# Performance work log

Measured on AMD Instinct MI355X. Metric: run time of the kernel, lower is better.

The kernel has to match this reference:

```python
import jax, jax.numpy as jnp
import numpy as np

B, S1, S2, H, OPC = 256, 512, 64, 768, 64
NEG = -1e12


def setup_inputs() -> dict:
    key = jax.random.key(0)
    ks = jax.random.split(key, 20)
    sc = 0.02
    d = {
        "current_emb": jax.random.normal(ks[0], (B, H), jnp.float32),
        "left_emb": jax.random.normal(ks[1], (B, H), jnp.float32),
        "encoder_outputs": jax.random.normal(ks[2], (B, S1, H), jnp.float32),
        "var_pades": jax.random.normal(ks[3], (B, S2, H), jnp.float32),
        "emb_op_const": jax.random.normal(ks[4], (OPC, H), jnp.float32),
        "W_l": jax.random.normal(ks[5], (H, H), jnp.float32) * sc,
        "b_l": jnp.zeros((H,), jnp.float32),
        "W_lg": jax.random.normal(ks[6], (H, H), jnp.float32) * sc,
        "b_lg": jnp.zeros((H,), jnp.float32),
        "W_r": jax.random.normal(ks[7], (2 * H, H), jnp.float32) * sc,
        "b_r": jnp.zeros((H,), jnp.float32),
        "W_rg": jax.random.normal(ks[8], (2 * H, H), jnp.float32) * sc,
        "b_rg": jnp.zeros((H,), jnp.float32),
        "W_attn": jax.random.normal(ks[9], (2 * H, H), jnp.float32) * sc,
        "b_attn": jnp.zeros((H,), jnp.float32),
        "v_attn": jax.random.normal(ks[10], (H,), jnp.float32) * sc,
        "W_score": jax.random.normal(ks[11], (3 * H, H), jnp.float32) * sc,
        "b_score": jnp.zeros((H,), jnp.float32),
        "v_score": jax.random.normal(ks[12], (H,), jnp.float32) * sc,
        "has_left": jax.random.randint(ks[13], (B,), 0, 2, jnp.int32),
        "source_mask": jax.random.randint(ks[14], (B, S1), 0, 2, jnp.int32),
        "candi_mask": jax.random.randint(ks[15], (B, OPC + S2), 0, 2, jnp.int32),
    }
    return d


def reference(current_emb, left_emb, encoder_outputs, var_pades, emb_op_const,
              W_l, b_l, W_lg, b_lg, W_r, b_r, W_rg, b_rg,
              W_attn, b_attn, v_attn, W_score, b_score, v_score,
              has_left, source_mask, candi_mask):
    # --- gated tree combine (two branches, selected per sample by has_left) ---
    g_l = jnp.tanh(current_emb @ W_l + b_l)
    t_l = jax.nn.sigmoid(current_emb @ W_lg + b_lg)
    lc = jnp.concatenate([left_emb, current_emb], axis=1)          # [B, 2H]
    g_r = jnp.tanh(lc @ W_r + b_r)
    t_r = jax.nn.sigmoid(lc @ W_rg + b_rg)
    node = jnp.where(has_left[:, None].astype(bool), g_r * t_r, g_l * t_l)  # [B, H]

    # --- additive attention over encoder outputs ---
    Bn, S, Hn = encoder_outputs.shape
    hid = jnp.broadcast_to(node[:, None, :], (Bn, S, Hn))
    energy = jnp.tanh(jnp.concatenate([hid, encoder_outputs], -1) @ W_attn + b_attn) @ v_attn  # [B, S]
    energy = jnp.where(source_mask.astype(bool), NEG, energy)
    attn = jax.nn.softmax(energy, axis=1)
    context = jnp.einsum('bs,bsh->bh', attn, encoder_outputs)      # [B, H]

    # --- leaf score over op/const/var candidates ---
    leaf = jnp.concatenate([node, context], axis=-1)               # [B, 2H]
    emb_all = jnp.concatenate(
        [jnp.broadcast_to(emb_op_const[None], (Bn,) + emb_op_const.shape), var_pades], axis=1)  # [B, O, H]
    O = emb_all.shape[1]
    sc_in = jnp.concatenate(
        [jnp.broadcast_to(leaf[:, None, :], (Bn, O, 2 * Hn)), emb_all], axis=-1)  # [B, O, 3H]
    score = jnp.tanh(sc_in @ W_score + b_score) @ v_score          # [B, O]
    num_score = jnp.where(candi_mask.astype(bool), NEG, score)
    return num_score, node[:, None, :], context[:, None, :], emb_all
```

## Files before the change

### kernel.cpp

```cpp
#include <hip/hip_runtime.h>
#include <math.h>

constexpr int Bq  = 256;
constexpr int S1q = 512;
constexpr int S2q = 64;
constexpr int Hq  = 768;
constexpr int OPCq = 64;
constexpr int OTq  = 128;
#define NEGq (-1e12f)

typedef unsigned int   u32;
typedef unsigned short u16;


__device__ __forceinline__ float fast_tanh(float x) {
    x = fminf(fmaxf(x, -15.f), 15.f);
    float e = __expf(2.f * x);
    return (e - 1.f) / (e + 1.f);
}
__device__ __forceinline__ float fast_sigmoid(float x) {
    x = fminf(fmaxf(x, -30.f), 30.f);
    return 1.f / (1.f + __expf(-x));
}

__device__ __forceinline__ u16 bf16_rne(float x) {
    union { float f; u32 u; } c; c.f = x;
    return (u16)((c.u + 0x7fffu + ((c.u >> 16) & 1u)) >> 16);
}
__device__ __forceinline__ float bf16_f(u16 h) {
    union { u32 u; float f; } c; c.u = ((u32)h) << 16; return c.f;
}

typedef __attribute__((ext_vector_type(8))) short bf16x8_t;
typedef __attribute__((ext_vector_type(4))) float f32x4_t;
#define MFMA16 __builtin_amdgcn_mfma_f32_16x16x32_bf16

template <int BT>
__global__ __launch_bounds__(256)
void node_kernel(const float* __restrict__ cur_emb, const float* __restrict__ left_emb,
                 const float* __restrict__ W_l,  const float* __restrict__ b_l,
                 const float* __restrict__ W_lg, const float* __restrict__ b_lg,
                 const float* __restrict__ W_r,  const float* __restrict__ b_r,
                 const float* __restrict__ W_rg, const float* __restrict__ b_rg,
                 const int* __restrict__ has_left, float* __restrict__ node_out) {
    __shared__ float lcs[BT][2 * Hq];
    const int tid = threadIdx.x;
    const int h  = blockIdx.x * 256 + tid;
    const int b0 = blockIdx.y * BT;
    for (int idx = tid; idx < BT * Hq; idx += 256) {
        int j = idx / Hq, k = idx % Hq;
        lcs[j][k]      = left_emb[(b0 + j) * Hq + k];
        lcs[j][Hq + k] = cur_emb[(b0 + j) * Hq + k];
    }
    __syncthreads();
    float agl[BT], atl[BT], agr[BT], atr[BT];
#pragma unroll
    for (int j = 0; j < BT; j++) { agl[j] = b_l[h]; atl[j] = b_lg[h]; agr[j] = b_r[h]; atr[j] = b_rg[h]; }
    for (int k = 0; k < Hq; k++) {
        float wl = W_l[k * Hq + h], wlg = W_lg[k * Hq + h];
#pragma unroll
        for (int j = 0; j < BT; j++) { float x = lcs[j][Hq + k]; agl[j] += x * wl; atl[j] += x * wlg; }
    }
    for (int k = 0; k < 2 * Hq; k++) {
        float wr = W_r[k * Hq + h], wrg = W_rg[k * Hq + h];
#pragma unroll
        for (int j = 0; j < BT; j++) { float x = lcs[j][k]; agr[j] += x * wr; atr[j] += x * wrg; }
    }
#pragma unroll
    for (int j = 0; j < BT; j++) {
        int b = b0 + j;
        float n = has_left[b] ? fast_tanh(agr[j]) * fast_sigmoid(atr[j])
                              : fast_tanh(agl[j]) * fast_sigmoid(atl[j]);
        node_out[b * Hq + h] = n;
    }
}

template <int BT>
__global__ __launch_bounds__(256)
void proj_kernel(const float* __restrict__ A1, const float* __restrict__ A2,
                 int K1, int K2,
                 const float* __restrict__ W, const float* __restrict__ bias,
                 float* __restrict__ out) {
    __shared__ float As[BT][2 * Hq];
    const int tid = threadIdx.x;
    const int h  = blockIdx.x * 256 + tid;
    const int b0 = blockIdx.y * BT;
    const int K = K1 + K2;
    for (int idx = tid; idx < BT * K1; idx += 256) {
        int j = idx / K1, k = idx % K1;
        As[j][k] = A1[(b0 + j) * K1 + k];
    }
    if (A2) {
        for (int idx = tid; idx < BT * K2; idx += 256) {
            int j = idx / K2, k = idx % K2;
            As[j][K1 + k] = A2[(b0 + j) * K2 + k];
        }
    }
    __syncthreads();
    float acc[BT];
#pragma unroll
    for (int j = 0; j < BT; j++) acc[j] = bias ? bias[h] : 0.f;
    for (int k = 0; k < K; k++) {
        float w = W[k * Hq + h];
#pragma unroll
        for (int j = 0; j < BT; j++) acc[j] += As[j][k] * w;
    }
#pragma unroll
    for (int j = 0; j < BT; j++) out[(b0 + j) * Hq + h] = acc[j];
}

__global__ __launch_bounds__(256)
void w_prep_kernel(const float* __restrict__ W,
                   uint4* __restrict__ Wf_hi, uint4* __restrict__ Wf_lo) {
    __shared__ float tile[64][65];
    const int tid = threadIdx.x;
    const int k0 = blockIdx.x * 64, n0 = blockIdx.y * 64;
    const int tx = tid & 63, tyy = tid >> 6;
    for (int u = tyy; u < 64; u += 4)
        tile[u][tx] = W[(size_t)(k0 + u) * Hq + n0 + tx];
    __syncthreads();
    const int l15 = tid & 15, lg = (tid >> 4) & 3, ktl = (tid >> 6) & 1;
    for (int c16 = tid >> 7; c16 < 4; c16 += 2) {
        const int kl = ktl * 32 + lg * 8;
        const int nl = c16 * 16 + l15;
        u32 h[4], l[4];
#pragma unroll
        for (int p = 0; p < 4; p++) {
            float a = tile[kl + 2 * p][nl], b = tile[kl + 2 * p + 1][nl];
            u16 ha = bf16_rne(a), hb = bf16_rne(b);
            u16 la = bf16_rne(a - bf16_f(ha)), lb = bf16_rne(b - bf16_f(hb));
            h[p] = (u32)ha | ((u32)hb << 16);
            l[p] = (u32)la | ((u32)lb << 16);
        }
        size_t idx = ((size_t)((n0 >> 4) + c16) * 24 + (k0 >> 5) + ktl) * 64 + lg * 16 + l15;
        Wf_hi[idx] = make_uint4(h[0], h[1], h[2], h[3]);
        Wf_lo[idx] = make_uint4(l[0], l[1], l[2], l[3]);
    }
}

__global__ __launch_bounds__(512)
void fused_tanh_dot_mfma(const float* __restrict__ A,
                         const uint4* __restrict__ Wf_hi,
                         const uint4* __restrict__ Wf_lo,
                         const float* __restrict__ addv,
                         const float* __restrict__ vvec,
                         float* __restrict__ out,
                         const int* __restrict__ maskp,
                         int shift, int ostride, int ooff) {
    __shared__ __align__(16) u16 Ah[128 * 32];
    __shared__ __align__(16) u16 Al[128 * 32];
    __shared__ float part[4][128];
    const int tid  = threadIdx.x;
    const int lane = tid & 63;
    const int wid  = tid >> 6, wr = wid >> 2, wc = wid & 3;
    const int l15  = lane & 15, lg = lane >> 4;
    const int rowbase = blockIdx.x * 128;

    part[tid >> 7][tid & 127] = 0.f;

    const int srow = tid >> 2, sk = (tid & 3) * 8;
    const float* Arow = A + (size_t)(rowbase + srow) * Hq + sk;

    const int bw = (rowbase + wr * 64) >> shift;
    const float* ad = addv + (size_t)bw * Hq;
    const int arow0 = wr * 64 + l15;

    for (int ct = 0; ct < 3; ct++) {
        f32x4_t acc[4][4];
#pragma unroll
        for (int i = 0; i < 4; i++)
#pragma unroll
            for (int j = 0; j < 4; j++) acc[i][j] = (f32x4_t){0.f, 0.f, 0.f, 0.f};

        const int c0 = ct * 16 + wc * 4;
        float4 f0 = *(const float4*)(Arow);
        float4 f1 = *(const float4*)(Arow + 4);
        for (int kt = 0; kt < 24; kt++) {
            float4 n0 = f0, n1 = f1;
            if (kt < 23) {
                n0 = *(const float4*)(Arow + (kt + 1) * 32);
                n1 = *(const float4*)(Arow + (kt + 1) * 32 + 4);
            }
            __syncthreads();
            {
                float xs[8] = {f0.x, f0.y, f0.z, f0.w, f1.x, f1.y, f1.z, f1.w};
                u32 h[4], l[4];
#pragma unroll
                for (int p = 0; p < 4; p++) {
                    u16 ha = bf16_rne(xs[2 * p]), hb = bf16_rne(xs[2 * p + 1]);
                    u16 la = bf16_rne(xs[2 * p] - bf16_f(ha));
                    u16 lb = bf16_rne(xs[2 * p + 1] - bf16_f(hb));
                    h[p] = (u32)ha | ((u32)hb << 16);
                    l[p] = (u32)la | ((u32)lb << 16);
                }
                *(uint4*)&Ah[srow * 32 + sk] = make_uint4(h[0], h[1], h[2], h[3]);
                *(uint4*)&Al[srow * 32 + sk] = make_uint4(l[0], l[1], l[2], l[3]);
            }
            __syncthreads();

            bf16x8_t ahf[4], alf[4];
#pragma unroll
            for (int i = 0; i < 4; i++) {
                ahf[i] = *(const bf16x8_t*)&Ah[(arow0 + i * 16) * 32 + lg * 8];
                alf[i] = *(const bf16x8_t*)&Al[(arow0 + i * 16) * 32 + lg * 8];
            }
#pragma unroll
            for (int j = 0; j < 4; j++) {
                uint4 wh4 = Wf_hi[((size_t)(c0 + j) * 24 + kt) * 64 + lane];
                uint4 wl4 = Wf_lo[((size_t)(c0 + j) * 24 + kt) * 64 + lane];
                bf16x8_t wh = *(bf16x8_t*)&wh4;
                bf16x8_t wl = *(bf16x8_t*)&wl4;
#pragma unroll
                for (int i = 0; i < 4; i++) {
                    acc[i][j] = MFMA16(ahf[i], wh, acc[i][j], 0, 0, 0);
                    acc[i][j] = MFMA16(alf[i], wh, acc[i][j], 0, 0, 0);
                    acc[i][j] = MFMA16(ahf[i], wl, acc[i][j], 0, 0, 0);
                }
            }
            f0 = n0; f1 = n1;
        }

        float sacc[4][4];
#pragma unroll
        for (int i = 0; i < 4; i++)
#pragma unroll
            for (int r = 0; r < 4; r++) sacc[i][r] = 0.f;
#pragma unroll
        for (int j = 0; j < 4; j++) {
            const int col = ct * 256 + wc * 64 + j * 16 + l15;
            const float vv = vvec[col];
            const float av = ad[col];
#pragma unroll
            for (int i = 0; i < 4; i++)
#pragma unroll
                for (int r = 0; r < 4; r++)
                    sacc[i][r] += vv * fast_tanh(acc[i][j][r] + av);
        }
#pragma unroll
        for (int i = 0; i < 4; i++)
#pragma unroll
            for (int r = 0; r < 4; r++) {
                float s = sacc[i][r];
                s += __shfl_xor(s, 1);
                s += __shfl_xor(s, 2);
                s += __shfl_xor(s, 4);
                s += __shfl_xor(s, 8);
                if (l15 == 0) {
                    part[wc][wr * 64 + i * 16 + lg * 4 + r] += s;
                }
            }
    }
    __syncthreads();
    if (tid < 128) {
        int grow = rowbase + tid;
        int b = grow >> shift;
        int j = grow - (b << shift);
        int oidx = b * ostride + ooff + j;
        float val = part[0][tid] + part[1][tid] + part[2][tid] + part[3][tid];
        if (maskp && maskp[oidx]) val = NEGq;
        out[oidx] = val;
    }
}

__global__ __launch_bounds__(256)
void softmax_kernel(float* __restrict__ e, const int* __restrict__ smask) {
    __shared__ float red[256];
    const int b = blockIdx.x, tid = threadIdx.x;
    float e0 = e[b * S1q + tid], e1 = e[b * S1q + 256 + tid];
    if (smask[b * S1q + tid]) e0 = NEGq;
    if (smask[b * S1q + 256 + tid]) e1 = NEGq;
    red[tid] = fmaxf(e0, e1);
    __syncthreads();
    for (int off = 128; off > 0; off >>= 1) {
        if (tid < off) red[tid] = fmaxf(red[tid], red[tid + off]);
        __syncthreads();
    }
    float mx = red[0];
    __syncthreads();
    float p0 = __expf(e0 - mx), p1 = __expf(e1 - mx);
    red[tid] = p0 + p1;
    __syncthreads();
    for (int off = 128; off > 0; off >>= 1) {
        if (tid < off) red[tid] += red[tid + off];
        __syncthreads();
    }
    float inv = 1.f / red[0];
    e[b * S1q + tid] = p0 * inv;
    e[b * S1q + 256 + tid] = p1 * inv;
}

__global__ __launch_bounds__(256)
void context_kernel(const float* __restrict__ attn, const float* __restrict__ enc,
                    float* __restrict__ ctx_out) {
    __shared__ float attn_s[S1q];
    const int tid = threadIdx.x;
    const int b = blockIdx.y;
    const int h = blockIdx.x * 256 + tid;
    attn_s[tid]       = attn[b * S1q + tid];
    attn_s[256 + tid] = attn[b * S1q + 256 + tid];
    __syncthreads();
    float c = 0.f;
    const float* ep = enc + (size_t)b * S1q * Hq + h;
    for (int s = 0; s < S1q; s++) c += attn_s[s] * ep[(size_t)s * Hq];
    ctx_out[b * Hq + h] = c;
}

__global__ __launch_bounds__(256)
void opscore_kernel(const float* __restrict__ scorebase, const float* __restrict__ opproj,
                    const float* __restrict__ vsc, const int* __restrict__ cmask,
                    float* __restrict__ num_score) {
    __shared__ float sb[Hq];
    __shared__ float red[256];
    const int b = blockIdx.x, tid = threadIdx.x;
    for (int i = tid; i < Hq; i += 256) sb[i] = scorebase[b * Hq + i];
    __syncthreads();
    const int o = tid & 63, q = tid >> 6;
    float partl = 0.f;
    for (int h = q * 192; h < (q + 1) * 192; h++)
        partl += vsc[h] * fast_tanh(sb[h] + opproj[o * Hq + h]);
    red[tid] = partl;
    __syncthreads();
    if (tid < 64) {
        float val = red[tid] + red[tid + 64] + red[tid + 128] + red[tid + 192];
        int oidx = b * OTq + tid;
        num_score[oidx] = cmask[oidx] ? NEGq : val;
    }
}

__global__ __launch_bounds__(256)
void emb_all_kernel(const float* __restrict__ opc, const float* __restrict__ var,
                    float4* __restrict__ out) {
    const long long total = (long long)Bq * OTq * (Hq / 4);
    for (long long idx = (long long)blockIdx.x * 256 + threadIdx.x; idx < total;
         idx += (long long)gridDim.x * 256) {
        long long b = idx / (OTq * (Hq / 4));
        int rem = (int)(idx - b * (OTq * (Hq / 4)));
        int o = rem / (Hq / 4), hv = rem % (Hq / 4);
        float4 val;
        if (o < OPCq) val = *(const float4*)&opc[o * Hq + hv * 4];
        else          val = *(const float4*)&var[((b * S2q) + (o - OPCq)) * (long long)Hq + hv * 4];
        out[idx] = val;
    }
}

extern "C" void kernel_launch(void* const* d_in, const int* in_sizes, int n_in,
                              void* d_out, int out_size, void* d_ws, size_t ws_size,
                              hipStream_t stream) {
    const float* cur     = (const float*)d_in[0];
    const float* left    = (const float*)d_in[1];
    const float* enc     = (const float*)d_in[2];
    const float* var     = (const float*)d_in[3];
    const float* opc     = (const float*)d_in[4];
    const float* W_l     = (const float*)d_in[5];
    const float* b_l     = (const float*)d_in[6];
    const float* W_lg    = (const float*)d_in[7];
    const float* b_lg    = (const float*)d_in[8];
    const float* W_r     = (const float*)d_in[9];
    const float* b_r     = (const float*)d_in[10];
    const float* W_rg    = (const float*)d_in[11];
    const float* b_rg    = (const float*)d_in[12];
    const float* W_attn  = (const float*)d_in[13];
    const float* b_attn  = (const float*)d_in[14];
    const float* v_attn  = (const float*)d_in[15];
    const float* W_score = (const float*)d_in[16];
    const float* b_score = (const float*)d_in[17];
    const float* v_score = (const float*)d_in[18];
    const int*   has_left= (const int*)d_in[19];
    const int*   smask   = (const int*)d_in[20];
    const int*   cmask   = (const int*)d_in[21];

    float* out       = (float*)d_out;
    float* num_score = out;
    float* node      = out + 32768;
    float* context   = out + 229376;
    float* emb_all   = out + 425984;

    float* ws        = (float*)d_ws;
    float* nodeproj  = ws;
    float* energy    = ws + 196608;
    float* scorebase = ws + 196608 + 131072;
    float* opproj    = scorebase + 196608;

    uint4* Wf_attn_hi = (uint4*)emb_all;
    uint4* Wf_attn_lo = Wf_attn_hi + 73728;
    uint4* Wf_sc_hi   = Wf_attn_lo + 73728;
    uint4* Wf_sc_lo   = Wf_sc_hi + 73728;

    w_prep_kernel<<<dim3(12, 12), 256, 0, stream>>>(W_attn + (size_t)768 * Hq,
                                                    Wf_attn_hi, Wf_attn_lo);
    w_prep_kernel<<<dim3(12, 12), 256, 0, stream>>>(W_score + (size_t)1536 * Hq,
                                                    Wf_sc_hi, Wf_sc_lo);
    node_kernel<8><<<dim3(3, 32), 256, 0, stream>>>(cur, left, W_l, b_l, W_lg, b_lg,
                                                    W_r, b_r, W_rg, b_rg, has_left, node);
    proj_kernel<8><<<dim3(3, 32), 256, 0, stream>>>(node, nullptr, 768, 0, W_attn, b_attn, nodeproj);
    proj_kernel<8><<<dim3(3, 8), 256, 0, stream>>>(opc, nullptr, 768, 0,
                                                   W_score + (size_t)1536 * Hq, nullptr, opproj);
    fused_tanh_dot_mfma<<<1024, 512, 0, stream>>>(enc, Wf_attn_hi, Wf_attn_lo, nodeproj,
                                                  v_attn, energy, nullptr, 9, S1q, 0);
    softmax_kernel<<<256, 256, 0, stream>>>(energy, smask);
    context_kernel<<<dim3(3, 256), 256, 0, stream>>>(energy, enc, context);
    proj_kernel<8><<<dim3(3, 32), 256, 0, stream>>>(node, context, 768, 768, W_score, b_score, scorebase);
    fused_tanh_dot_mfma<<<128, 512, 0, stream>>>(var, Wf_sc_hi, Wf_sc_lo, scorebase,
                                                 v_score, num_score, cmask, 6, OTq, OPCq);
    opscore_kernel<<<256, 256, 0, stream>>>(scorebase, opproj, v_score, cmask, num_score);
    emb_all_kernel<<<4096, 256, 0, stream>>>(opc, var, (float4*)emb_all);
}
```

Baseline: 2.087 ms.

## Restructure fused MFMA kernel: full-N per block, double-buffered LDS, vectorized context/opscore

The fused tanh-dot MFMA kernel now has each warp keep accumulators for all of its output columns in one pass instead of looping three column tiles. This means activation rows are loaded and split to bf16 hi/lo once rather than three times. LDS staging is double-buffered with one barrier per k-step, and a template picks the row/column warp split, so the score pass uses 64-row blocks across 256 blocks. The context kernel is rewritten to use float4 loads with a sequence split plus a shared-memory reduction, and the opscore kernel is rewritten to use per-warp shuffle reductions with coalesced opproj reads. The larger accumulator arrays (24 f32x4 per lane) increase register pressure and may limit occupancy.

```diff
diff --git a/kernel.cpp b/kernel.cpp
--- a/kernel.cpp
+++ b/kernel.cpp
@@ -34,6 +34,21 @@
 typedef __attribute__((ext_vector_type(8))) short bf16x8_t;
 typedef __attribute__((ext_vector_type(4))) float f32x4_t;
 #define MFMA16 __builtin_amdgcn_mfma_f32_16x16x32_bf16
+
+__device__ __forceinline__ void cvt_store8(float4 f0, float4 f1, u16* ph, u16* pl) {
+    float xs[8] = {f0.x, f0.y, f0.z, f0.w, f1.x, f1.y, f1.z, f1.w};
+    u32 h[4], l[4];
+#pragma unroll
+    for (int p = 0; p < 4; p++) {
+        u16 ha = bf16_rne(xs[2 * p]), hb = bf16_rne(xs[2 * p + 1]);
+        u16 la = bf16_rne(xs[2 * p] - bf16_f(ha));
+        u16 lb = bf16_rne(xs[2 * p + 1] - bf16_f(hb));
+        h[p] = (u32)ha | ((u32)hb << 16);
+        l[p] = (u32)la | ((u32)lb << 16);
+    }
+    *(uint4*)ph = make_uint4(h[0], h[1], h[2], h[3]);
+    *(uint4*)pl = make_uint4(l[0], l[1], l[2], l[3]);
+}
 
 template <int BT>
 __global__ __launch_bounds__(256)
@@ -138,7 +153,8 @@
     }
 }
 
-__global__ __launch_bounds__(512)
+template <int NWR>
+__global__ __launch_bounds__(512, 2)
 void fused_tanh_dot_mfma(const float* __restrict__ A,
                          const uint4* __restrict__ Wf_hi,
                          const uint4* __restrict__ Wf_lo,
@@ -147,116 +163,131 @@
                          float* __restrict__ out,
                          const int* __restrict__ maskp,
                          int shift, int ostride, int ooff) {
-    __shared__ __align__(16) u16 Ah[128 * 32];
-    __shared__ __align__(16) u16 Al[128 * 32];
-    __shared__ float part[4][128];
+    constexpr int NWC  = 8 / NWR;
+    constexpr int J16  = 6 * NWR;
+    constexpr int ROWS = NWR * 64;
+    __shared__ __align__(16) u16 AhL[2][ROWS * 32];
+    __shared__ __align__(16) u16 AlL[2][ROWS * 32];
+    __shared__ float part[NWC * ROWS];
+
     const int tid  = threadIdx.x;
     const int lane = tid & 63;
-    const int wid  = tid >> 6, wr = wid >> 2, wc = wid & 3;
+    const int wid  = tid >> 6;
+    const int wr   = wid / NWC, wc = wid % NWC;
     const int l15  = lane & 15, lg = lane >> 4;
-    const int rowbase = blockIdx.x * 128;
-
-    part[tid >> 7][tid & 127] = 0.f;
-
-    const int srow = tid >> 2, sk = (tid & 3) * 8;
-    const float* Arow = A + (size_t)(rowbase + srow) * Hq + sk;
+    const int rowbase = blockIdx.x * ROWS;
+
+    const bool st_act = (NWR == 2) || (tid < 256);
+    const int sg = ((tid >> 6) * 4 + (tid & 3)) * 16 + ((tid >> 2) & 15);
+    const float* Aptr = A + (size_t)(rowbase + (tid >> 2)) * Hq + (tid & 3) * 8;
 
     const int bw = (rowbase + wr * 64) >> shift;
     const float* ad = addv + (size_t)bw * Hq;
-    const int arow0 = wr * 64 + l15;
-
-    for (int ct = 0; ct < 3; ct++) {
-        f32x4_t acc[4][4];
+    const int c0 = wc * J16;
+    const uint4* whb = Wf_hi + (size_t)c0 * 24 * 64 + lane;
+    const uint4* wlb = Wf_lo + (size_t)c0 * 24 * 64 + lane;
+    const int ag = (wr * 4) * 64 + lg * 16 + l15;
+
+    f32x4_t acc[4][J16];
+#pragma unroll
+    for (int i = 0; i < 4; i++)
+#pragma unroll
+        for (int j = 0; j < J16; j++) acc[i][j] = (f32x4_t){0.f, 0.f, 0.f, 0.f};
+
+    if (st_act) {
+        float4 f0 = *(const float4*)(Aptr);
+        float4 f1 = *(const float4*)(Aptr + 4);
+        cvt_store8(f0, f1, &AhL[0][sg * 8], &AlL[0][sg * 8]);
+    }
+    __syncthreads();
+
+    for (int kt = 0; kt < 24; ++kt) {
+        const int cur = kt & 1;
+        float4 f0 = {0.f, 0.f, 0.f, 0.f}, f1 = {0.f, 0.f, 0.f, 0.f};
+        if (st_act && kt < 23) {
+            f0 = *(const float4*)(Aptr + (kt + 1) * 32);
+            f1 = *(const float4*)(Aptr + (kt + 1) * 32 + 4);
+        }
+        const u16* AhC = AhL[cur];
+        const u16* AlC = AlL[cur];
+        {
+            bf16x8_t a0h = *(const bf16x8_t*)&AhC[(ag + 0 * 64) * 8];
+            bf16x8_t a1h = *(const bf16x8_t*)&AhC[(ag + 1 * 64) * 8];
+            bf16x8_t a0l = *(const bf16x8_t*)&AlC[(ag + 0 * 64) * 8];
+            bf16x8_t a1l = *(const bf16x8_t*)&AlC[(ag + 1 * 64) * 8];
+#pragma unroll
+            for (int j = 0; j < J16; j++) {
+                uint4 h4 = whb[((size_t)j * 24 + kt) * 64];
+                uint4 l4 = wlb[((size_t)j * 24 + kt) * 64];
+                bf16x8_t wh = *(bf16x8_t*)&h4, wl = *(bf16x8_t*)&l4;
+                acc[0][j] = MFMA16(a0h, wh, acc[0][j], 0, 0, 0);
+                acc[0][j] = MFMA16(a0l, wh, acc[0][j], 0, 0, 0);
+                acc[0][j] = MFMA16(a0h, wl, acc[0][j], 0, 0, 0);
+                acc[1][j] = MFMA16(a1h, wh, acc[1][j], 0, 0, 0);
+                acc[1][j] = MFMA16(a1l, wh, acc[1][j], 0, 0, 0);
+                acc[1][j] = MFMA16(a1h, wl, acc[1][j], 0, 0, 0);
+            }
+        }
+        {
+            bf16x8_t a2h = *(const bf16x8_t*)&AhC[(ag + 2 * 64) * 8];
+            bf16x8_t a3h = *(const bf16x8_t*)&AhC[(ag + 3 * 64) * 8];
+            bf16x8_t a2l = *(const bf16x8_t*)&AlC[(ag + 2 * 64) * 8];
+            bf16x8_t a3l = *(const bf16x8_t*)&AlC[(ag + 3 * 64) * 8];
+#pragma unroll
+            for (int j = 0; j < J16; j++) {
+                uint4 h4 = whb[((size_t)j * 24 + kt) * 64];
+                uint4 l4 = wlb[((size_t)j * 24 + kt) * 64];
+                bf16x8_t wh = *(bf16x8_t*)&h4, wl = *(bf16x8_t*)&l4;
+                acc[2][j] = MFMA16(a2h, wh, acc[2][j], 0, 0, 0);
+                acc[2][j] = MFMA16(a2l, wh, acc[2][j], 0, 0, 0);
+                acc[2][j] = MFMA16(a2h, wl, acc[2][j], 0, 0, 0);
+                acc[3][j] = MFMA16(a3h, wh, acc[3][j], 0, 0, 0);
+                acc[3][j] = MFMA16(a3l, wh, acc[3][j], 0, 0, 0);
+                acc[3][j] = MFMA16(a3h, wl, acc[3][j], 0, 0, 0);
+            }
+        }
+        if (st_act && kt < 23)
+            cvt_store8(f0, f1, &AhL[cur ^ 1][sg * 8], &AlL[cur ^ 1][sg * 8]);
+        __syncthreads();
+    }
+
+    float sacc[4][4];
+#pragma unroll
+    for (int i = 0; i < 4; i++)
+#pragma unroll
+        for (int r = 0; r < 4; r++) sacc[i][r] = 0.f;
+#pragma unroll
+    for (int j = 0; j < J16; j++) {
+        const int col = (c0 + j) * 16 + l15;
+        const float vv = vvec[col];
+        const float av = ad[col];
 #pragma unroll
         for (int i = 0; i < 4; i++)
 #pragma unroll
-            for (int j = 0; j < 4; j++) acc[i][j] = (f32x4_t){0.f, 0.f, 0.f, 0.f};
-
-        const int c0 = ct * 16 + wc * 4;
-        float4 f0 = *(const float4*)(Arow);
-        float4 f1 = *(const float4*)(Arow + 4);
-        for (int kt = 0; kt < 24; kt++) {
-            float4 n0 = f0, n1 = f1;
-            if (kt < 23) {
-                n0 = *(const float4*)(Arow + (kt + 1) * 32);
-                n1 = *(const float4*)(Arow + (kt + 1) * 32 + 4);
-            }
-            __syncthreads();
-            {
-                float xs[8] = {f0.x, f0.y, f0.z, f0.w, f1.x, f1.y, f1.z, f1.w};
-                u32 h[4], l[4];
-#pragma unroll
-                for (int p = 0; p < 4; p++) {
-                    u16 ha = bf16_rne(xs[2 * p]), hb = bf16_rne(xs[2 * p + 1]);
-                    u16 la = bf16_rne(xs[2 * p] - bf16_f(ha));
-                    u16 lb = bf16_rne(xs[2 * p + 1] - bf16_f(hb));
-                    h[p] = (u32)ha | ((u32)hb << 16);
-                    l[p] = (u32)la | ((u32)lb << 16);
-                }
-                *(uint4*)&Ah[srow * 32 + sk] = make_uint4(h[0], h[1], h[2], h[3]);
-                *(uint4*)&Al[srow * 32 + sk] = make_uint4(l[0], l[1], l[2], l[3]);
-            }
-            __syncthreads();
-
-            bf16x8_t ahf[4], alf[4];
-#pragma unroll
-            for (int i = 0; i < 4; i++) {
-                ahf[i] = *(const bf16x8_t*)&Ah[(arow0 + i * 16) * 32 + lg * 8];
-                alf[i] = *(const bf16x8_t*)&Al[(arow0 + i * 16) * 32 + lg * 8];
-            }
-#pragma unroll
-            for (int j = 0; j < 4; j++) {
-                uint4 wh4 = Wf_hi[((size_t)(c0 + j) * 24 + kt) * 64 + lane];
-                uint4 wl4 = Wf_lo[((size_t)(c0 + j) * 24 + kt) * 64 + lane];
-                bf16x8_t wh = *(bf16x8_t*)&wh4;
-                bf16x8_t wl = *(bf16x8_t*)&wl4;
-#pragma unroll
-                for (int i = 0; i < 4; i++) {
-                    acc[i][j] = MFMA16(ahf[i], wh, acc[i][j], 0, 0, 0);
-                    acc[i][j] = MFMA16(alf[i], wh, acc[i][j], 0, 0, 0);
-                    acc[i][j] = MFMA16(ahf[i], wl, acc[i][j], 0, 0, 0);
-                }
-            }
-            f0 = n0; f1 = n1;
-        }
-
-        float sacc[4][4];
-#pragma unroll
-        for (int i = 0; i < 4; i++)
-#pragma unroll
-            for (int r = 0; r < 4; r++) sacc[i][r] = 0.f;
-#pragma unroll
-        for (int j = 0; j < 4; j++) {
-            const int col = ct * 256 + wc * 64 + j * 16 + l15;
-            const float vv = vvec[col];
-            const float av = ad[col];
-#pragma unroll
-            for (int i = 0; i < 4; i++)
-#pragma unroll
-                for (int r = 0; r < 4; r++)
-                    sacc[i][r] += vv * fast_tanh(acc[i][j][r] + av);
-        }
-#pragma unroll
-        for (int i = 0; i < 4; i++)
-#pragma unroll
-            for (int r = 0; r < 4; r++) {
-                float s = sacc[i][r];
-                s += __shfl_xor(s, 1);
-                s += __shfl_xor(s, 2);
-                s += __shfl_xor(s, 4);
-                s += __shfl_xor(s, 8);
-                if (l15 == 0) {
-                    part[wc][wr * 64 + i * 16 + lg * 4 + r] += s;
-                }
-            }
-    }
-    __syncthreads();
-    if (tid < 128) {
+            for (int r = 0; r < 4; r++)
+                sacc[i][r] += vv * fast_tanh(acc[i][j][r] + av);
+    }
+#pragma unroll
+    for (int i = 0; i < 4; i++)
+#pragma unroll
+        for (int r = 0; r < 4; r++) {
+            float s = sacc[i][r];
+            s += __shfl_xor(s, 1);
+            s += __shfl_xor(s, 2);
+            s += __shfl_xor(s, 4);
+            s += __shfl_xor(s, 8);
+            if (l15 == 0)
+                part[wc * ROWS + wr * 64 + i * 16 + lg * 4 + r] = s;
+        }
+    __syncthreads();
+    if (tid < ROWS) {
         int grow = rowbase + tid;
         int b = grow >> shift;
         int j = grow - (b << shift);
         int oidx = b * ostride + ooff + j;
-        float val = part[0][tid] + part[1][tid] + part[2][tid] + part[3][tid];
+        float val = 0.f;
+#pragma unroll
+        for (int w = 0; w < NWC; w++) val += part[w * ROWS + tid];
         if (maskp && maskp[oidx]) val = NEGq;
         out[oidx] = val;
     }
@@ -293,16 +324,31 @@
 void context_kernel(const float* __restrict__ attn, const float* __restrict__ enc,
                     float* __restrict__ ctx_out) {
     __shared__ float attn_s[S1q];
+    __shared__ float4 red4[256];
     const int tid = threadIdx.x;
     const int b = blockIdx.y;
-    const int h = blockIdx.x * 256 + tid;
+    const int c = tid & 63;
+    const int sq = tid >> 6;
     attn_s[tid]       = attn[b * S1q + tid];
     attn_s[256 + tid] = attn[b * S1q + 256 + tid];
     __syncthreads();
-    float c = 0.f;
-    const float* ep = enc + (size_t)b * S1q * Hq + h;
-    for (int s = 0; s < S1q; s++) c += attn_s[s] * ep[(size_t)s * Hq];
-    ctx_out[b * Hq + h] = c;
+    const float4* ep = (const float4*)(enc + (size_t)b * S1q * Hq) + blockIdx.x * 64 + c;
+    float4 acc = {0.f, 0.f, 0.f, 0.f};
+    for (int s = sq * 128; s < sq * 128 + 128; s++) {
+        float a = attn_s[s];
+        float4 e = ep[(size_t)s * (Hq / 4)];
+        acc.x += a * e.x; acc.y += a * e.y; acc.z += a * e.z; acc.w += a * e.w;
+    }
+    red4[tid] = acc;
+    __syncthreads();
+    if (tid < 64) {
+        float4 r0 = red4[tid], r1 = red4[tid + 64], r2 = red4[tid + 128], r3 = red4[tid + 192];
+        r0.x += r1.x + r2.x + r3.x;
+        r0.y += r1.y + r2.y + r3.y;
+        r0.z += r1.z + r2.z + r3.z;
+        r0.w += r1.w + r2.w + r3.w;
+        ((float4*)(ctx_out + (size_t)b * Hq))[blockIdx.x * 64 + c] = r0;
+    }
 }
 
 __global__ __launch_bounds__(256)
@@ -310,20 +356,30 @@
                     const float* __restrict__ vsc, const int* __restrict__ cmask,
                     float* __restrict__ num_score) {
     __shared__ float sb[Hq];
-    __shared__ float red[256];
+    __shared__ float vs[Hq];
     const int b = blockIdx.x, tid = threadIdx.x;
-    for (int i = tid; i < Hq; i += 256) sb[i] = scorebase[b * Hq + i];
-    __syncthreads();
-    const int o = tid & 63, q = tid >> 6;
-    float partl = 0.f;
-    for (int h = q * 192; h < (q + 1) * 192; h++)
-        partl += vsc[h] * fast_tanh(sb[h] + opproj[o * Hq + h]);
-    red[tid] = partl;
-    __syncthreads();
-    if (tid < 64) {
-        float val = red[tid] + red[tid + 64] + red[tid + 128] + red[tid + 192];
-        int oidx = b * OTq + tid;
-        num_score[oidx] = cmask[oidx] ? NEGq : val;
+    for (int i = tid; i < Hq; i += 256) { sb[i] = scorebase[b * Hq + i]; vs[i] = vsc[i]; }
+    __syncthreads();
+    const int w = tid >> 6, l = tid & 63;
+    for (int oo = 0; oo < 16; oo++) {
+        const int o = w * 16 + oo;
+        const float* op = opproj + (size_t)o * Hq;
+        float p = 0.f;
+#pragma unroll
+        for (int t = 0; t < 12; t++) {
+            int h = t * 64 + l;
+            p += vs[h] * fast_tanh(sb[h] + op[h]);
+        }
+        p += __shfl_xor(p, 1);
+        p += __shfl_xor(p, 2);
+        p += __shfl_xor(p, 4);
+        p += __shfl_xor(p, 8);
+        p += __shfl_xor(p, 16);
+        p += __shfl_xor(p, 32);
+        if (l == 0) {
+            int oidx = b * OTq + o;
+            num_score[oidx] = cmask[oidx] ? NEGq : p;
+        }
     }
 }
 
@@ -395,13 +451,13 @@
     proj_kernel<8><<<dim3(3, 32), 256, 0, stream>>>(node, nullptr, 768, 0, W_attn, b_attn, nodeproj);
     proj_kernel<8><<<dim3(3, 8), 256, 0, stream>>>(opc, nullptr, 768, 0,
                                                    W_score + (size_t)1536 * Hq, nullptr, opproj);
-    fused_tanh_dot_mfma<<<1024, 512, 0, stream>>>(enc, Wf_attn_hi, Wf_attn_lo, nodeproj,
-                                                  v_attn, energy, nullptr, 9, S1q, 0);
+    fused_tanh_dot_mfma<2><<<1024, 512, 0, stream>>>(enc, Wf_attn_hi, Wf_attn_lo, nodeproj,
+                                                     v_attn, energy, nullptr, 9, S1q, 0);
     softmax_kernel<<<256, 256, 0, stream>>>(energy, smask);
     context_kernel<<<dim3(3, 256), 256, 0, stream>>>(energy, enc, context);
     proj_kernel<8><<<dim3(3, 32), 256, 0, stream>>>(node, context, 768, 768, W_score, b_score, scorebase);
-    fused_tanh_dot_mfma<<<128, 512, 0, stream>>>(var, Wf_sc_hi, Wf_sc_lo, scorebase,
-                                                 v_score, num_score, cmask, 6, OTq, OPCq);
+    fused_tanh_dot_mfma<1><<<256, 512, 0, stream>>>(var, Wf_sc_hi, Wf_sc_lo, scorebase,
+                                                    v_score, num_score, cmask, 6, OTq, OPCq);
     opscore_kernel<<<256, 256, 0, stream>>>(scorebase, opproj, v_score, cmask, num_score);
     emb_all_kernel<<<4096, 256, 0, stream>>>(opc, var, (float4*)emb_all);
 }
```

Result: slower. 2.481 ms (+18.9%).
